# Kernel tuning notes

Measured on AMD Instinct MI355X. Metric: run time of the kernel, lower is better.

## Reference

```python
import jax, jax.numpy as jnp
import numpy as np

TEMP = 0.05
DIAG_PENALTY = 1e12
EPS = 1e-8  # matches torch F.cosine_similarity eps


def setup_inputs() -> dict:
    key = jax.random.key(0)
    x = jax.random.normal(key, (8192, 768), dtype=jnp.float32)
    return {"x": x}


def reference(x):
    n = x.shape[0]
    # labels: swap adjacent pairs -> i - (i%2)*2 + 1  (i.e. i XOR 1)
    idx = jnp.arange(n)
    labels = idx - (idx % 2) * 2 + 1
    # cosine similarity matrix via normalize + GEMM (same math as broadcasted
    # F.cosine_similarity: dot(x_i, x_j) / (max(||x_i||,eps) * max(||x_j||,eps)))
    norms = jnp.maximum(jnp.linalg.norm(x, axis=-1, keepdims=True), EPS)
    xn = x / norms
    sim = xn @ xn.T                                   # [N, N]
    sim = sim - jnp.eye(n, dtype=sim.dtype) * DIAG_PENALTY
    logits = sim / TEMP
    # mean cross-entropy with stable log-softmax
    logp = jax.nn.log_softmax(logits, axis=-1)
    loss = -jnp.mean(jnp.take_along_axis(logp, labels[:, None], axis=-1))
    return loss
```

## Files before the change

### kernel.cpp

```cpp
#include <hip/hip_runtime.h>
#include <hip/hip_bf16.h>

#define N 8192
#define D 768
#define TEMP_INV 20.0f
#define NTILES 2080

typedef __attribute__((ext_vector_type(4))) float f32x4;
typedef __attribute__((ext_vector_type(4))) int i32x4;
typedef __attribute__((ext_vector_type(8))) int i32x8;

#define SCALE1 0x7F7F7F7F


__global__ __launch_bounds__(256) void norm_kernel(
    const float* __restrict__ x, unsigned char* __restrict__ xn,
    float* __restrict__ rowsum) {
  int t = threadIdx.x, w = t >> 6, lane = t & 63;
  int row = blockIdx.x * 4 + w;
  const float4* xr = (const float4*)(x + (size_t)row * D);
  float4 v[3];
  v[0] = xr[lane];
  v[1] = xr[lane + 64];
  v[2] = xr[lane + 128];
  float ss = 0.0f;
#pragma unroll
  for (int i = 0; i < 3; ++i)
    ss += v[i].x * v[i].x + v[i].y * v[i].y + v[i].z * v[i].z + v[i].w * v[i].w;
#pragma unroll
  for (int m = 32; m; m >>= 1) ss += __shfl_xor(ss, m);
  float inv = 1.0f / fmaxf(sqrtf(ss), 1e-8f);
  unsigned int* xo = (unsigned int*)(xn + (size_t)row * D);
#pragma unroll
  for (int i = 0; i < 3; ++i) {
    int p = __builtin_amdgcn_cvt_pk_fp8_f32(v[i].x * inv, v[i].y * inv, 0, false);
    p = __builtin_amdgcn_cvt_pk_fp8_f32(v[i].z * inv, v[i].w * inv, p, true);
    xo[lane + 64 * i] = p;
  }
  if (t < 4) rowsum[blockIdx.x * 4 + t] = 0.0f;
}

__global__ __launch_bounds__(256, 3) void sim_kernel(
    const unsigned char* __restrict__ xn, float* __restrict__ rowsum,
    float* __restrict__ pos) {
  int L = blockIdx.x;
  float f = (129.0f - sqrtf(16641.0f - 8.0f * (float)L)) * 0.5f;
  int bi = (int)f;
  while (64 * (bi + 1) - ((bi + 1) * bi) / 2 <= L) ++bi;
  while (64 * bi - (bi * (bi - 1)) / 2 > L) --bi;
  int bj = bi + (L - (64 * bi - (bi * (bi - 1)) / 2));

  __shared__ __align__(16) unsigned char As[128 * 128];
  __shared__ __align__(16) unsigned char Bs[128 * 128];

  int t = threadIdx.x;
  int w = t >> 6, lane = t & 63;
  int q = lane >> 4, cl = lane & 15;
  int wm = w >> 1, wn = w & 1;

  f32x4 acc[4][4] = {};

  int ulog = (((t & 7) ^ ((t >> 3) & 7))) * 16;
  const unsigned char* Ab = xn + (size_t)(bi * 128 + (t >> 3)) * D + ulog;
  const unsigned char* Bb = xn + (size_t)(bj * 128 + (t >> 3)) * D + ulog;

  int off0 = ((2 * q) ^ (cl & 7)) * 16;

  for (int kc = 0; kc < 6; ++kc) {
    int k0 = kc * 128;
#pragma unroll
    for (int rr = 0; rr < 4; ++rr) {
      __builtin_amdgcn_global_load_lds(
          (const __attribute__((address_space(1))) unsigned int*)(Ab + (size_t)(rr * 32) * D + k0),
          (__attribute__((address_space(3))) unsigned int*)(As + rr * 4096 + t * 16), 16, 0, 0);
      __builtin_amdgcn_global_load_lds(
          (const __attribute__((address_space(1))) unsigned int*)(Bb + (size_t)(rr * 32) * D + k0),
          (__attribute__((address_space(3))) unsigned int*)(Bs + rr * 4096 + t * 16), 16, 0, 0);
    }
    __syncthreads();

    union Frag { i32x8 v8; struct { i32x4 lo, hi; } p; };
    Frag a[4], b[4];
#pragma unroll
    for (int m = 0; m < 4; ++m) {
      const unsigned char* base = As + (wm * 64 + m * 16 + cl) * 128;
      a[m].p.lo = *(const i32x4*)(base + off0);
      a[m].p.hi = *(const i32x4*)(base + (off0 ^ 16));
    }
#pragma unroll
    for (int n = 0; n < 4; ++n) {
      const unsigned char* base = Bs + (wn * 64 + n * 16 + cl) * 128;
      b[n].p.lo = *(const i32x4*)(base + off0);
      b[n].p.hi = *(const i32x4*)(base + (off0 ^ 16));
    }
#pragma unroll
    for (int m = 0; m < 4; ++m)
#pragma unroll
      for (int n = 0; n < 4; ++n)
        acc[m][n] = __builtin_amdgcn_mfma_scale_f32_16x16x128_f8f6f4(
            a[m].v8, b[n].v8, acc[m][n], 0, 0, 0, SCALE1, 0, SCALE1);
    __syncthreads();
  }

  int gi0 = bi * 128 + wm * 64;
  int gj0 = bj * 128 + wn * 64;

  float rowp[4][4] = {};
  float colp[4] = {};

  if (bi == bj) {
#pragma unroll
    for (int m = 0; m < 4; ++m)
#pragma unroll
      for (int n = 0; n < 4; ++n)
#pragma unroll
        for (int r = 0; r < 4; ++r) {
          float s = acc[m][n][r];
          int row = gi0 + m * 16 + q * 4 + r;
          int col = gj0 + n * 16 + cl;
          float e = __expf(TEMP_INV * s - 20.0f);
          if (col == row) e = 0.0f;
          if (col == (row ^ 1)) pos[row] = TEMP_INV * s;
          rowp[m][r] += e;
        }
  } else {
#pragma unroll
    for (int m = 0; m < 4; ++m)
#pragma unroll
      for (int n = 0; n < 4; ++n)
#pragma unroll
        for (int r = 0; r < 4; ++r) {
          float e = __expf(TEMP_INV * acc[m][n][r] - 20.0f);
          rowp[m][r] += e;
          colp[n] += e;
        }
  }

#pragma unroll
  for (int m = 0; m < 4; ++m)
#pragma unroll
    for (int r = 0; r < 4; ++r) {
      float v = rowp[m][r];
      v += __shfl_xor(v, 1);
      v += __shfl_xor(v, 2);
      v += __shfl_xor(v, 4);
      v += __shfl_xor(v, 8);
      if (cl == 0) atomicAdd(&rowsum[gi0 + m * 16 + q * 4 + r], v);
    }
  if (bi != bj) {
#pragma unroll
    for (int n = 0; n < 4; ++n) {
      float v = colp[n];
      v += __shfl_xor(v, 16);
      v += __shfl_xor(v, 32);
      if (q == 0) atomicAdd(&rowsum[gj0 + n * 16 + cl], v);
    }
  }
}

__global__ __launch_bounds__(1024) void loss_kernel(
    const float* __restrict__ rowsum, const float* __restrict__ pos,
    float* __restrict__ out) {
  int t = threadIdx.x;
  const float4* r4 = (const float4*)rowsum;
  const float4* p4 = (const float4*)pos;
  float acc = 0.0f;
#pragma unroll
  for (int it = 0; it < 2; ++it) {
    int i = t + it * 1024;
    float4 r = r4[i], p = p4[i];
    acc += 80.0f + __logf(r.x) + __logf(r.y) + __logf(r.z) + __logf(r.w)
           - p.x - p.y - p.z - p.w;
  }
#pragma unroll
  for (int m = 32; m; m >>= 1) acc += __shfl_xor(acc, m);
  __shared__ float wsum[16];
  if ((t & 63) == 0) wsum[t >> 6] = acc;
  __syncthreads();
  if (t == 0) {
    float tot = 0.0f;
#pragma unroll
    for (int i = 0; i < 16; ++i) tot += wsum[i];
    out[0] = tot / (float)N;
  }
}

extern "C" void kernel_launch(void* const* d_in, const int* in_sizes, int n_in,
                              void* d_out, int out_size, void* d_ws, size_t ws_size,
                              hipStream_t stream) {
  const float* x = (const float*)d_in[0];
  float* rowsum = (float*)d_ws;
  float* pos = rowsum + N;
  unsigned char* xn = (unsigned char*)(rowsum + 2 * N + 16);

  norm_kernel<<<N / 4, 256, 0, stream>>>(x, xn, rowsum);
  sim_kernel<<<NTILES, 256, 0, stream>>>(xn, rowsum, pos);
  loss_kernel<<<1, 1024, 0, stream>>>(rowsum, pos, (float*)d_out);
}
```

Before: 129.0 us.

## Remap triangular tile order into XCD-local super-tiles and raise occupancy

Replaces the closed-form triangular block index with a mapping that first spreads block IDs across the 8 XCDs (260 tiles per XCD) and then walks 8x8 super-tiles of the upper triangle. Neighbouring blocks on the same XCD therefore reuse the same A/B row panels in that XCD's L2. LDS is now declared as i32x4 arrays indexed by 16-byte units, and launch bounds allow 4 blocks per CU instead of 3. The cost is a small table lookup and loop per block, plus possible register spills under the tighter occupancy bound.

```diff
diff --git a/kernel.cpp b/kernel.cpp
--- a/kernel.cpp
+++ b/kernel.cpp
@@ -40,18 +40,41 @@
   if (t < 4) rowsum[blockIdx.x * 4 + t] = 0.0f;
 }
 
-__global__ __launch_bounds__(256, 3) void sim_kernel(
+__global__ __launch_bounds__(256, 4) void sim_kernel(
     const unsigned char* __restrict__ xn, float* __restrict__ rowsum,
     float* __restrict__ pos) {
-  int L = blockIdx.x;
-  float f = (129.0f - sqrtf(16641.0f - 8.0f * (float)L)) * 0.5f;
-  int bi = (int)f;
-  while (64 * (bi + 1) - ((bi + 1) * bi) / 2 <= L) ++bi;
-  while (64 * bi - (bi * (bi - 1)) / 2 > L) --bi;
-  int bj = bi + (L - (64 * bi - (bi * (bi - 1)) / 2));
-
-  __shared__ __align__(16) unsigned char As[128 * 128];
-  __shared__ __align__(16) unsigned char Bs[128 * 128];
+  static const short stbase[37] = {
+      0, 36, 100, 164, 228, 292, 356, 420,
+      484, 520, 584, 648, 712, 776, 840,
+      904, 940, 1004, 1068, 1132, 1196,
+      1260, 1296, 1360, 1424, 1488,
+      1552, 1588, 1652, 1716,
+      1780, 1816, 1880,
+      1944, 1980,
+      2044, 2080};
+  static const char sti[36] = {0,0,0,0,0,0,0,0, 1,1,1,1,1,1,1, 2,2,2,2,2,2,
+                               3,3,3,3,3, 4,4,4,4, 5,5,5, 6,6, 7};
+  static const char stj[36] = {0,1,2,3,4,5,6,7, 1,2,3,4,5,6,7, 2,3,4,5,6,7,
+                               3,4,5,6,7, 4,5,6,7, 5,6,7, 6,7, 7};
+  int b = blockIdx.x;
+  int p = 260 * (b & 7) + (b >> 3);
+  int s = 0;
+  while ((int)stbase[s + 1] <= p) ++s;
+  int wofs = p - stbase[s];
+  int SI = sti[s], SJ = stj[s];
+  int bi, bj;
+  if (SI == SJ) {
+    int di = 0, cum = 0;
+    while (wofs >= cum + (8 - di)) { cum += 8 - di; ++di; }
+    bi = SI * 8 + di;
+    bj = SI * 8 + di + (wofs - cum);
+  } else {
+    bi = SI * 8 + (wofs >> 3);
+    bj = SJ * 8 + (wofs & 7);
+  }
+
+  __shared__ i32x4 As4[128 * 8];
+  __shared__ i32x4 Bs4[128 * 8];
 
   int t = threadIdx.x;
   int w = t >> 6, lane = t & 63;
@@ -64,7 +87,8 @@
   const unsigned char* Ab = xn + (size_t)(bi * 128 + (t >> 3)) * D + ulog;
   const unsigned char* Bb = xn + (size_t)(bj * 128 + (t >> 3)) * D + ulog;
 
-  int off0 = ((2 * q) ^ (cl & 7)) * 16;
+  int u0 = (2 * q) ^ (cl & 7);
+  int u1 = u0 ^ 1;
 
   for (int kc = 0; kc < 6; ++kc) {
     int k0 = kc * 128;
@@ -72,33 +96,33 @@
     for (int rr = 0; rr < 4; ++rr) {
       __builtin_amdgcn_global_load_lds(
           (const __attribute__((address_space(1))) unsigned int*)(Ab + (size_t)(rr * 32) * D + k0),
-          (__attribute__((address_space(3))) unsigned int*)(As + rr * 4096 + t * 16), 16, 0, 0);
+          (__attribute__((address_space(3))) unsigned int*)(As4 + rr * 256 + t), 16, 0, 0);
       __builtin_amdgcn_global_load_lds(
           (const __attribute__((address_space(1))) unsigned int*)(Bb + (size_t)(rr * 32) * D + k0),
-          (__attribute__((address_space(3))) unsigned int*)(Bs + rr * 4096 + t * 16), 16, 0, 0);
+          (__attribute__((address_space(3))) unsigned int*)(Bs4 + rr * 256 + t), 16, 0, 0);
     }
     __syncthreads();
 
-    union Frag { i32x8 v8; struct { i32x4 lo, hi; } p; };
-    Frag a[4], b[4];
+    union Frag { i32x8 v8; struct { i32x4 lo, hi; } pr; };
+    Frag a[4], bb[4];
 #pragma unroll
     for (int m = 0; m < 4; ++m) {
-      const unsigned char* base = As + (wm * 64 + m * 16 + cl) * 128;
-      a[m].p.lo = *(const i32x4*)(base + off0);
-      a[m].p.hi = *(const i32x4*)(base + (off0 ^ 16));
+      int rowb = (wm * 64 + m * 16 + cl) * 8;
+      a[m].pr.lo = As4[rowb + u0];
+      a[m].pr.hi = As4[rowb + u1];
     }
 #pragma unroll
     for (int n = 0; n < 4; ++n) {
-      const unsigned char* base = Bs + (wn * 64 + n * 16 + cl) * 128;
-      b[n].p.lo = *(const i32x4*)(base + off0);
-      b[n].p.hi = *(const i32x4*)(base + (off0 ^ 16));
+      int rowb = (wn * 64 + n * 16 + cl) * 8;
+      bb[n].pr.lo = Bs4[rowb + u0];
+      bb[n].pr.hi = Bs4[rowb + u1];
     }
 #pragma unroll
     for (int m = 0; m < 4; ++m)
 #pragma unroll
       for (int n = 0; n < 4; ++n)
         acc[m][n] = __builtin_amdgcn_mfma_scale_f32_16x16x128_f8f6f4(
-            a[m].v8, b[n].v8, acc[m][n], 0, 0, 0, SCALE1, 0, SCALE1);
+            a[m].v8, bb[n].v8, acc[m][n], 0, 0, 0, SCALE1, 0, SCALE1);
     __syncthreads();
   }
 
@@ -115,12 +139,12 @@
       for (int n = 0; n < 4; ++n)
 #pragma unroll
         for (int r = 0; r < 4; ++r) {
-          float s = acc[m][n][r];
+          float sv = acc[m][n][r];
           int row = gi0 + m * 16 + q * 4 + r;
           int col = gj0 + n * 16 + cl;
-          float e = __expf(TEMP_INV * s - 20.0f);
+          float e = __expf(TEMP_INV * sv - 20.0f);
           if (col == row) e = 0.0f;
-          if (col == (row ^ 1)) pos[row] = TEMP_INV * s;
+          if (col == (row ^ 1)) pos[row] = TEMP_INV * sv;
           rowp[m][r] += e;
         }
   } else {
@@ -168,9 +192,9 @@
 #pragma unroll
   for (int it = 0; it < 2; ++it) {
     int i = t + it * 1024;
-    float4 r = r4[i], p = p4[i];
+    float4 r = r4[i], pp = p4[i];
     acc += 80.0f + __logf(r.x) + __logf(r.y) + __logf(r.z) + __logf(r.w)
-           - p.x - p.y - p.z - p.w;
+           - pp.x - pp.y - pp.z - pp.w;
   }
 #pragma unroll
   for (int m = 32; m; m >>= 1) acc += __shfl_xor(acc, m);
```

After: 125.0 us. 1.03x faster.
